# Optimization experiments

Measured on AMD Instinct MI355X. Metric: run time of the kernel, lower is better.

Reference implementation:

```python
import jax, jax.numpy as jnp
import numpy as np

B, N, C = 2, 2048, 1024
H = 16
D = C // H
HID = 4 * C
EPS = 1e-5


def layernorm(x, g, b):
    mu = jnp.mean(x, axis=-1, keepdims=True)
    var = jnp.var(x, axis=-1, keepdims=True)
    return (x - mu) * jax.lax.rsqrt(var + EPS) * g + b


def setup_inputs() -> dict:
    key = jax.random.key(0)
    ks = jax.random.split(key, 8)
    s = lambda fan_in: 1.0 / np.sqrt(fan_in)
    return {
        "x": jax.random.normal(ks[0], (B, N, C), dtype=jnp.float32),
        "ln1_g": jnp.ones((C,), jnp.float32),
        "ln1_b": jnp.zeros((C,), jnp.float32),
        "w_qkv": jax.random.normal(ks[1], (C, 3 * C), jnp.float32) * s(C),
        "w_proj": jax.random.normal(ks[2], (C, C), jnp.float32) * s(C),
        "b_proj": jnp.zeros((C,), jnp.float32),
        "ln2_g": jnp.ones((C,), jnp.float32),
        "ln2_b": jnp.zeros((C,), jnp.float32),
        "w_fc1": jax.random.normal(ks[3], (C, HID), jnp.float32) * s(C),
        "b_fc1": jnp.zeros((HID,), jnp.float32),
        "w_fc2": jax.random.normal(ks[4], (HID, C), jnp.float32) * s(HID),
        "b_fc2": jnp.zeros((C,), jnp.float32),
        "metadata": 0,
        "thw_shape": 2048,
    }


def reference(x, ln1_g, ln1_b, w_qkv, w_proj, b_proj, ln2_g, ln2_b,
              w_fc1, b_fc1, w_fc2, b_fc2, metadata, thw_shape):
    scale = 1.0 / np.sqrt(D)
    # --- attention branch (pre-norm) ---
    xn = layernorm(x, ln1_g, ln1_b)
    qkv = (xn @ w_qkv).reshape(B, N, 3, H, D)
    q = jnp.transpose(qkv[:, :, 0], (0, 2, 1, 3))  # [B,H,N,D]
    k = jnp.transpose(qkv[:, :, 1], (0, 2, 1, 3))
    v = jnp.transpose(qkv[:, :, 2], (0, 2, 1, 3))
    attn = jax.nn.softmax(jnp.einsum('bhnd,bhmd->bhnm', q, k) * scale, axis=-1)
    o = jnp.einsum('bhnm,bhmd->bhnd', attn, v)
    o = jnp.transpose(o, (0, 2, 1, 3)).reshape(B, N, C)
    x = x + (o @ w_proj + b_proj)
    # --- MLP branch (pre-norm) ---
    xn2 = layernorm(x, ln2_g, ln2_b)
    h = jax.nn.gelu(xn2 @ w_fc1 + b_fc1, approximate=False)  # torch GELU = exact erf
    x = x + (h @ w_fc2 + b_fc2)
    return x
```

## Files before the change

### kernel.cpp

```cpp
#include <hip/hip_runtime.h>

#define B_   2
#define N_   2048
#define C_   1024
#define H_   16
#define D_   64
#define HID_ 4096
#define M_   (B_ * N_)

typedef __attribute__((ext_vector_type(8))) short bf16x8;
typedef __attribute__((ext_vector_type(4))) short short4v;
typedef __attribute__((ext_vector_type(4))) float f32x4;

__device__ __forceinline__ unsigned short f2bf(float f) {
  unsigned int u = __builtin_bit_cast(unsigned int, f);
  u += 0x7fffu + ((u >> 16) & 1u);
  return (unsigned short)(u >> 16);
}

__device__ __forceinline__ void gl2lds16(const void* g, void* l) {
  __builtin_amdgcn_global_load_lds(
      (const __attribute__((address_space(1))) unsigned int*)g,
      (__attribute__((address_space(3))) unsigned int*)l, 16, 0, 0);
}

__global__ __launch_bounds__(256) void ln_kernel(const float* __restrict__ x,
                                                 const float* __restrict__ g,
                                                 const float* __restrict__ bta,
                                                 unsigned short* __restrict__ out) {
  int row  = blockIdx.x * 4 + (threadIdx.x >> 6);
  int lane = threadIdx.x & 63;
  const float* xr = x + (size_t)row * C_;
  float4 v[4];
  float s1 = 0.f, s2 = 0.f;
#pragma unroll
  for (int j = 0; j < 4; j++) {
    v[j] = *(const float4*)(xr + j * 256 + lane * 4);
    s1 += v[j].x + v[j].y + v[j].z + v[j].w;
    s2 += v[j].x * v[j].x + v[j].y * v[j].y + v[j].z * v[j].z + v[j].w * v[j].w;
  }
#pragma unroll
  for (int m = 1; m < 64; m <<= 1) { s1 += __shfl_xor(s1, m); s2 += __shfl_xor(s2, m); }
  float mu  = s1 * (1.0f / C_);
  float var = s2 * (1.0f / C_) - mu * mu;
  float rs  = rsqrtf(var + 1e-5f);
#pragma unroll
  for (int j = 0; j < 4; j++) {
    const float4 gv = *(const float4*)(g + j * 256 + lane * 4);
    const float4 bv = *(const float4*)(bta + j * 256 + lane * 4);
    ushort4 o;
    o.x = f2bf((v[j].x - mu) * rs * gv.x + bv.x);
    o.y = f2bf((v[j].y - mu) * rs * gv.y + bv.y);
    o.z = f2bf((v[j].z - mu) * rs * gv.z + bv.z);
    o.w = f2bf((v[j].w - mu) * rs * gv.w + bv.w);
    *(ushort4*)(out + (size_t)row * C_ + j * 256 + lane * 4) = o;
  }
}

__global__ __launch_bounds__(256) void wtrans_kernel(const float* __restrict__ W,
                                                     unsigned short* __restrict__ Wt,
                                                     int K, int N) {
  __shared__ float t[32][33];
  int n0 = blockIdx.x * 32, k0 = blockIdx.y * 32;
  int tx = threadIdx.x, ty = threadIdx.y;
#pragma unroll
  for (int j = 0; j < 4; j++)
    t[ty + j * 8][tx] = W[(size_t)(k0 + ty + j * 8) * N + n0 + tx];
  __syncthreads();
#pragma unroll
  for (int j = 0; j < 4; j++)
    Wt[(size_t)(n0 + ty + j * 8) * K + k0 + tx] = f2bf(t[tx][ty + j * 8]);
}

__global__ __launch_bounds__(256) void vtrans_kernel(const unsigned short* __restrict__ v,
                                                     unsigned short* __restrict__ vt) {
  __shared__ unsigned short t[32][33];
  int bh = blockIdx.z;
  int n0 = blockIdx.x * 32, d0 = blockIdx.y * 32;
  const unsigned short* src = v + (size_t)bh * N_ * D_;
  unsigned short* dst = vt + (size_t)bh * D_ * N_;
  int tx = threadIdx.x, ty = threadIdx.y;
#pragma unroll
  for (int j = 0; j < 4; j++)
    t[ty + j * 8][tx] = src[(size_t)(n0 + ty + j * 8) * D_ + d0 + tx];
  __syncthreads();
#pragma unroll
  for (int j = 0; j < 4; j++)
    dst[(size_t)(d0 + ty + j * 8) * N_ + n0 + tx] = t[tx][ty + j * 8];
}

template <int MODE, int BN>
__global__ __launch_bounds__(256) void gemm_kernel(
    const unsigned short* __restrict__ A,
    const unsigned short* __restrict__ Wt,
    const float* __restrict__ bias,
    const float* __restrict__ resid,
    float* __restrict__ outf,
    unsigned short* __restrict__ outb0,
    unsigned short* __restrict__ outb1,
    unsigned short* __restrict__ outb2,
    int M, int N, int K) {
  constexpr int MT = (BN == 128) ? 4 : 2;
  __shared__ __align__(16) short As[128][64];
  __shared__ __align__(16) short Bs[BN][64];
  int tid = threadIdx.x;
  int w = tid >> 6, lane = tid & 63, r = lane & 15, quad = lane >> 4;
  int rowbase = (BN == 128) ? (w >> 1) * 64 : w * 32;
  int colbase = (BN == 128) ? (w & 1) * 64 : 0;
  int bM = blockIdx.y * 128, bN = blockIdx.x * BN;

  int srow   = (w << 3) + (lane >> 3);
  int schunk = (lane & 7) ^ ((lane >> 3) & 7);
  const unsigned short* aP = A  + (size_t)(bM + srow) * K + schunk * 8;
  const unsigned short* bP = Wt + (size_t)(bN + srow) * K + schunk * 8;

  int pc0 = (quad ^ (r & 7)) * 8;

  f32x4 acc[MT][4];
#pragma unroll
  for (int i = 0; i < MT; i++)
#pragma unroll
    for (int j = 0; j < 4; j++) acc[i][j] = f32x4{0.f, 0.f, 0.f, 0.f};

  for (int k0 = 0; k0 < K; k0 += 64) {
    __syncthreads();
#pragma unroll
    for (int p = 0; p < 4; p++)
      gl2lds16(aP + (size_t)(p * 32) * K + k0, &As[p * 32 + (w << 3)][0]);
#pragma unroll
    for (int p = 0; p < BN / 32; p++)
      gl2lds16(bP + (size_t)(p * 32) * K + k0, &Bs[p * 32 + (w << 3)][0]);
    __syncthreads();
#pragma unroll
    for (int kh = 0; kh < 2; kh++) {
      int pc = pc0 ^ (kh * 32);
      bf16x8 af[MT], bfr[4];
#pragma unroll
      for (int mt = 0; mt < MT; mt++)
        af[mt] = *(const bf16x8*)&As[rowbase + mt * 16 + r][pc];
#pragma unroll
      for (int nt = 0; nt < 4; nt++)
        bfr[nt] = *(const bf16x8*)&Bs[colbase + nt * 16 + r][pc];
#pragma unroll
      for (int mt = 0; mt < MT; mt++)
#pragma unroll
        for (int nt = 0; nt < 4; nt++)
          acc[mt][nt] = __builtin_amdgcn_mfma_f32_16x16x32_bf16(af[mt], bfr[nt], acc[mt][nt], 0, 0, 0);
    }
  }

#pragma unroll
  for (int mt = 0; mt < MT; mt++) {
#pragma unroll
    for (int nt = 0; nt < 4; nt++) {
#pragma unroll
      for (int i = 0; i < 4; i++) {
        int gm = bM + rowbase + mt * 16 + quad * 4 + i;
        int gn = bN + colbase + nt * 16 + r;
        float val = acc[mt][nt][i];
        if (MODE == 0) {
          int s = gn >> 10, c = gn & 1023;
          int hh = c >> 6, d = c & 63;
          int b = gm >> 11, n = gm & 2047;
          size_t di = ((size_t)(b * H_ + hh) * N_ + n) * D_ + d;
          unsigned short bvv = f2bf(s == 0 ? val * 0.125f : val);
          (s == 0 ? outb0 : (s == 1 ? outb1 : outb2))[di] = bvv;
        } else if (MODE == 1) {
          outf[(size_t)gm * N + gn] = val + bias[gn] + resid[(size_t)gm * N + gn];
        } else {
          float t = val + bias[gn];
          float gl = 0.5f * t * (1.0f + erff(t * 0.70710678118f));
          outb0[(size_t)gm * N + gn] = f2bf(gl);
        }
      }
    }
  }
}

__global__ __launch_bounds__(256) void attn_kernel(const unsigned short* __restrict__ qb,
                                                   const unsigned short* __restrict__ kb,
                                                   const unsigned short* __restrict__ vtb,
                                                   unsigned short* __restrict__ ob) {
  __shared__ __align__(16) short Ks[128][64];
  __shared__ __align__(16) short Vts[64][128];
  int tid = threadIdx.x;
  int w = tid >> 6, lane = tid & 63, r = lane & 15, quad = lane >> 4;
  int bh = blockIdx.x >> 4, qt = blockIdx.x & 15;
  const unsigned short* qh  = qb  + (size_t)bh * N_ * D_;
  const unsigned short* kh  = kb  + (size_t)bh * N_ * D_;
  const unsigned short* vth = vtb + (size_t)bh * D_ * N_;

  bf16x8 qf[2][2];
#pragma unroll
  for (int mt = 0; mt < 2; mt++)
#pragma unroll
    for (int ks = 0; ks < 2; ks++)
      qf[mt][ks] = *(const bf16x8*)(qh + (size_t)(qt * 128 + w * 32 + mt * 16 + r) * D_ + ks * 32 + quad * 8);

  float mst[2] = {-1e30f, -1e30f}, lst[2] = {0.f, 0.f};
  f32x4 oacc[2][4];
#pragma unroll
  for (int mt = 0; mt < 2; mt++)
#pragma unroll
    for (int nt = 0; nt < 4; nt++) oacc[mt][nt] = f32x4{0.f, 0.f, 0.f, 0.f};

  int krow   = (w << 3) + (lane >> 3);
  int kchunk = (lane & 7) ^ ((lane >> 3) & 7);
  const unsigned short* kP = kh + (size_t)krow * D_ + kchunk * 8;
  int vrow   = (w << 2) + (lane >> 4);
  int vchunk = (lane & 15) ^ (vrow & 7);
  const unsigned short* vP = vth + (size_t)vrow * N_ + vchunk * 8;

  short* Plw = &Ks[0][0] + w * 2048;
  int swz = (r & 7);

  for (int t = 0; t < 16; t++) {
    __syncthreads();
#pragma unroll
    for (int p = 0; p < 4; p++)
      gl2lds16(kP + (size_t)(t * 128 + p * 32) * D_, &Ks[p * 32 + (w << 3)][0]);
#pragma unroll
    for (int p = 0; p < 4; p++)
      gl2lds16(vP + (size_t)(p * 16) * N_ + t * 128, &Vts[p * 16 + (w << 2)][0]);
    __syncthreads();

    f32x4 sacc[2][8];
#pragma unroll
    for (int mt = 0; mt < 2; mt++)
#pragma unroll
      for (int nt = 0; nt < 8; nt++) sacc[mt][nt] = f32x4{0.f, 0.f, 0.f, 0.f};
#pragma unroll
    for (int ks = 0; ks < 2; ks++) {
#pragma unroll
      for (int nt = 0; nt < 8; nt++) {
        bf16x8 kfr = *(const bf16x8*)&Ks[nt * 16 + r][((ks * 4 + quad) ^ swz) * 8];
#pragma unroll
        for (int mt = 0; mt < 2; mt++)
          sacc[mt][nt] = __builtin_amdgcn_mfma_f32_16x16x32_bf16(kfr, qf[mt][ks], sacc[mt][nt], 0, 0, 0);
      }
    }

    float alpha[2];
#pragma unroll
    for (int mt = 0; mt < 2; mt++) {
      float tm = -1e30f;
#pragma unroll
      for (int nt = 0; nt < 8; nt++)
#pragma unroll
        for (int i = 0; i < 4; i++) tm = fmaxf(tm, sacc[mt][nt][i]);
      tm = fmaxf(tm, __shfl_xor(tm, 16));
      tm = fmaxf(tm, __shfl_xor(tm, 32));
      float mnew = fmaxf(mst[mt], tm);
      alpha[mt] = __expf(mst[mt] - mnew);
      mst[mt] = mnew;
      float rs = 0.f;
#pragma unroll
      for (int nt = 0; nt < 8; nt++)
#pragma unroll
        for (int i = 0; i < 4; i++) {
          float p = __expf(sacc[mt][nt][i] - mnew);
          sacc[mt][nt][i] = p;
          rs += p;
        }
      rs += __shfl_xor(rs, 16);
      rs += __shfl_xor(rs, 32);
      lst[mt] = lst[mt] * alpha[mt] + rs;
#pragma unroll
      for (int i = 0; i < 4; i++) {
        float av = __shfl(alpha[mt], (lane & 48) | (quad * 4 + i));
#pragma unroll
        for (int nt = 0; nt < 4; nt++) oacc[mt][nt][i] *= av;
      }
    }

    __syncthreads();

#pragma unroll
    for (int mt = 0; mt < 2; mt++) {
#pragma unroll
      for (int nt = 0; nt < 8; nt++) {
        short4v pk;
        pk[0] = (short)f2bf(sacc[mt][nt][0]);
        pk[1] = (short)f2bf(sacc[mt][nt][1]);
        pk[2] = (short)f2bf(sacc[mt][nt][2]);
        pk[3] = (short)f2bf(sacc[mt][nt][3]);
        *(short4v*)&Plw[r * 128 + (((nt * 2 + (quad >> 1)) ^ swz) * 8) + (quad & 1) * 4] = pk;
      }
      asm volatile("" ::: "memory");
#pragma unroll
      for (int ks = 0; ks < 4; ks++) {
        bf16x8 pfr = *(const bf16x8*)&Plw[r * 128 + ((ks * 4 + quad) ^ swz) * 8];
#pragma unroll
        for (int nt2 = 0; nt2 < 4; nt2++) {
          bf16x8 vfr = *(const bf16x8*)&Vts[nt2 * 16 + r][((ks * 4 + quad) ^ swz) * 8];
          oacc[mt][nt2] = __builtin_amdgcn_mfma_f32_16x16x32_bf16(pfr, vfr, oacc[mt][nt2], 0, 0, 0);
        }
      }
      asm volatile("" ::: "memory");
    }
  }

  int bb = bh >> 4, hh = bh & 15;
#pragma unroll
  for (int mt = 0; mt < 2; mt++) {
#pragma unroll
    for (int i = 0; i < 4; i++) {
      float li = __shfl(lst[mt], (lane & 48) | (quad * 4 + i));
      float inv = 1.0f / li;
      int row = qt * 128 + w * 32 + mt * 16 + quad * 4 + i;
#pragma unroll
      for (int nt2 = 0; nt2 < 4; nt2++) {
        int d = nt2 * 16 + r;
        ob[((size_t)bb * N_ + row) * C_ + hh * D_ + d] = f2bf(oacc[mt][nt2][i] * inv);
      }
    }
  }
}

extern "C" void kernel_launch(void* const* d_in, const int* in_sizes, int n_in,
                              void* d_out, int out_size, void* d_ws, size_t ws_size,
                              hipStream_t stream) {
  const float* x     = (const float*)d_in[0];
  const float* ln1g  = (const float*)d_in[1];
  const float* ln1b  = (const float*)d_in[2];
  const float* wqkv  = (const float*)d_in[3];
  const float* wproj = (const float*)d_in[4];
  const float* bproj = (const float*)d_in[5];
  const float* ln2g  = (const float*)d_in[6];
  const float* ln2b  = (const float*)d_in[7];
  const float* wfc1  = (const float*)d_in[8];
  const float* bfc1  = (const float*)d_in[9];
  const float* wfc2  = (const float*)d_in[10];
  const float* bfc2  = (const float*)d_in[11];
  float* out = (float*)d_out;

  const size_t MB = 1u << 20;
  if (ws_size < 88 * MB) return;
  char* w = (char*)d_ws;
  unsigned short* xn    = (unsigned short*)(w + 0 * MB);
  unsigned short* qbuf  = (unsigned short*)(w + 8 * MB);
  unsigned short* kbuf  = (unsigned short*)(w + 16 * MB);
  unsigned short* vbuf  = (unsigned short*)(w + 24 * MB);
  unsigned short* hbuf  = (unsigned short*)(w + 0 * MB);
  unsigned short* obuf  = (unsigned short*)(w + 32 * MB);
  float*          x2    = (float*)         (w + 40 * MB);
  unsigned short* xn2   = (unsigned short*)(w + 56 * MB);
  unsigned short* vtb   = (unsigned short*)(w + 56 * MB);
  unsigned short* wqkvt = (unsigned short*)(w + 64 * MB);
  unsigned short* wprjt = (unsigned short*)(w + 70 * MB);
  unsigned short* wfc1t = (unsigned short*)(w + 72 * MB);
  unsigned short* wfc2t = (unsigned short*)(w + 80 * MB);

  dim3 tb(32, 8);
  ln_kernel<<<M_ / 4, 256, 0, stream>>>(x, ln1g, ln1b, xn);
  wtrans_kernel<<<dim3(3 * C_ / 32, C_ / 32), tb, 0, stream>>>(wqkv, wqkvt, C_, 3 * C_);
  wtrans_kernel<<<dim3(C_ / 32, C_ / 32), tb, 0, stream>>>(wproj, wprjt, C_, C_);
  wtrans_kernel<<<dim3(HID_ / 32, C_ / 32), tb, 0, stream>>>(wfc1, wfc1t, C_, HID_);
  wtrans_kernel<<<dim3(C_ / 32, HID_ / 32), tb, 0, stream>>>(wfc2, wfc2t, HID_, C_);

  gemm_kernel<0, 128><<<dim3(3 * C_ / 128, M_ / 128), 256, 0, stream>>>(
      xn, wqkvt, nullptr, nullptr, nullptr, qbuf, kbuf, vbuf, M_, 3 * C_, C_);
  vtrans_kernel<<<dim3(N_ / 32, D_ / 32, B_ * H_), tb, 0, stream>>>(vbuf, vtb);
  attn_kernel<<<B_ * H_ * (N_ / 128), 256, 0, stream>>>(qbuf, kbuf, vtb, obuf);
  gemm_kernel<1, 64><<<dim3(C_ / 64, M_ / 128), 256, 0, stream>>>(
      obuf, wprjt, bproj, x, x2, nullptr, nullptr, nullptr, M_, C_, C_);
  ln_kernel<<<M_ / 4, 256, 0, stream>>>(x2, ln2g, ln2b, xn2);
  gemm_kernel<2, 128><<<dim3(HID_ / 128, M_ / 128), 256, 0, stream>>>(
      xn2, wfc1t, bfc1, nullptr, nullptr, hbuf, nullptr, nullptr, M_, HID_, C_);
  gemm_kernel<1, 64><<<dim3(C_ / 64, M_ / 128), 256, 0, stream>>>(
      hbuf, wfc2t, bfc2, x2, out, nullptr, nullptr, nullptr, M_, C_, HID_);
}
```

Baseline: 385.8 us.

## Add 256x256-tile 8-wave GEMM with interleaved staging for QKV and FC1

Adds a new GEMM kernel that uses 256x256 output tiles with 512 threads, a double-buffered LDS layout with XOR swizzle, and a schedule that splits global-to-LDS loads into quarter-tiles interleaved with MFMA phases under raised wave priority. The QKV and FC1 projections switch to it. The goal is more data reuse per tile and better overlap of memory loads with matrix math. In exchange the grid gets much smaller (192 and 256 blocks), which can leave CUs underused on a 256-CU part, and register pressure is high with 128 accumulator floats per thread.

```diff
diff --git a/kernel.cpp b/kernel.cpp
--- a/kernel.cpp
+++ b/kernel.cpp
@@ -177,6 +177,175 @@
   }
 }
 
+template <int MODE>
+__global__ __launch_bounds__(512, 2) void gemm256_kernel(
+    const unsigned short* __restrict__ A,
+    const unsigned short* __restrict__ Wt,
+    const float* __restrict__ bias,
+    float* __restrict__ outf,
+    const float* __restrict__ resid,
+    unsigned short* __restrict__ outb0,
+    unsigned short* __restrict__ outb1,
+    unsigned short* __restrict__ outb2,
+    int M, int N, int K) {
+  __shared__ __align__(16) short As[2][256][64];
+  __shared__ __align__(16) short Bs[2][256][64];
+  const int tid = threadIdx.x;
+  const int w = tid >> 6, lane = tid & 63, r = lane & 15, quad = lane >> 4;
+  const int wr = w >> 2, wc = w & 3;
+  const int bN = blockIdx.x * 256, bM = blockIdx.y * 256;
+
+  const int srow   = (w << 3) + (lane >> 3);
+  const int schunk = (lane & 7) ^ ((lane >> 3) & 7);
+  const unsigned short* aSrc = A  + (size_t)(bM + srow) * K + schunk * 8;
+  const unsigned short* bSrc = Wt + (size_t)(bN + srow) * K + schunk * 8;
+  const int wrow = w << 3;
+
+  const int ntiles = K >> 6;
+  const int tmask  = ntiles - 1;
+
+#define STAGE_H(t, h)                                                            \
+  do {                                                                           \
+    int b_ = (t) & 1, tt_ = (t) & tmask;                                         \
+    if ((h) < 2) {                                                               \
+      const unsigned short* p_ = aSrc + (size_t)((h) * 128) * K + tt_ * 64;      \
+      gl2lds16(p_, &As[b_][(h) * 128 + wrow][0]);                                \
+      gl2lds16(p_ + (size_t)64 * K, &As[b_][(h) * 128 + 64 + wrow][0]);          \
+    } else {                                                                     \
+      const unsigned short* p_ = bSrc + (size_t)(((h) - 2) * 128) * K + tt_ * 64;\
+      gl2lds16(p_, &Bs[b_][((h) - 2) * 128 + wrow][0]);                          \
+      gl2lds16(p_ + (size_t)64 * K, &Bs[b_][((h) - 2) * 128 + 64 + wrow][0]);    \
+    }                                                                            \
+  } while (0)
+
+  f32x4 acc[8][4];
+#pragma unroll
+  for (int i = 0; i < 8; i++)
+#pragma unroll
+    for (int j = 0; j < 4; j++) acc[i][j] = f32x4{0.f, 0.f, 0.f, 0.f};
+
+  bf16x8 af[4][2];
+  bf16x8 bfr[4][2];
+
+#define RD_A(b, msub)                                                            \
+  {                                                                              \
+    _Pragma("unroll") for (int mt_ = 0; mt_ < 4; mt_++)                          \
+      _Pragma("unroll") for (int ks_ = 0; ks_ < 2; ks_++)                        \
+        af[mt_][ks_] = *(const bf16x8*)&As[b][wr * 128 + (msub) * 64 + mt_ * 16 + r] \
+                                          [((ks_ * 4 + quad) ^ (r & 7)) * 8];    \
+  }
+#define RD_B(b, nh)                                                              \
+  {                                                                              \
+    _Pragma("unroll") for (int nt_ = 0; nt_ < 2; nt_++)                          \
+      _Pragma("unroll") for (int ks_ = 0; ks_ < 2; ks_++)                        \
+        bfr[(nh) * 2 + nt_][ks_] =                                               \
+            *(const bf16x8*)&Bs[b][wc * 64 + (nh) * 32 + nt_ * 16 + r]           \
+                               [((ks_ * 4 + quad) ^ (r & 7)) * 8];               \
+  }
+#define MM_Q(msub, nh)                                                           \
+  {                                                                              \
+    _Pragma("unroll") for (int mt_ = 0; mt_ < 4; mt_++)                          \
+      _Pragma("unroll") for (int nt_ = 0; nt_ < 2; nt_++)                        \
+        _Pragma("unroll") for (int ks_ = 0; ks_ < 2; ks_++)                      \
+          acc[(msub) * 4 + mt_][(nh) * 2 + nt_] =                                \
+              __builtin_amdgcn_mfma_f32_16x16x32_bf16(                           \
+                  af[mt_][ks_], bfr[(nh) * 2 + nt_][ks_],                        \
+                  acc[(msub) * 4 + mt_][(nh) * 2 + nt_], 0, 0, 0);               \
+  }
+
+#define BARRIER() asm volatile("s_barrier" ::: "memory")
+#define WAITL()   asm volatile("s_waitcnt lgkmcnt(0)" ::: "memory")
+#define WAITV2()  asm volatile("s_waitcnt vmcnt(2)" ::: "memory")
+#define PRIO1()   __builtin_amdgcn_s_setprio(1)
+#define PRIO0()   __builtin_amdgcn_s_setprio(0)
+
+  STAGE_H(0, 0); STAGE_H(0, 1); STAGE_H(0, 2); STAGE_H(0, 3);
+  STAGE_H(1, 0);
+  WAITV2();
+  BARRIER();
+
+  const int niter = ntiles >> 1;
+  for (int i = 0; i < niter; i++) {
+    const int tc = 2 * i;
+    RD_A(0, 0); RD_B(0, 0);
+    STAGE_H(tc + 1, 1);
+    BARRIER(); WAITL();
+    PRIO1(); MM_Q(0, 0); PRIO0();
+    BARRIER();
+    RD_B(0, 1);
+    STAGE_H(tc + 1, 2);
+    BARRIER(); WAITL();
+    PRIO1(); MM_Q(0, 1); PRIO0();
+    BARRIER();
+    RD_A(0, 1);
+    STAGE_H(tc + 1, 3);
+    BARRIER(); WAITL();
+    PRIO1(); MM_Q(1, 1); PRIO0();
+    BARRIER();
+    STAGE_H(tc + 2, 0);
+    BARRIER(); WAITL();
+    PRIO1(); MM_Q(1, 0); PRIO0();
+    WAITV2();
+    BARRIER();
+    RD_A(1, 0); RD_B(1, 0);
+    STAGE_H(tc + 2, 1);
+    BARRIER(); WAITL();
+    PRIO1(); MM_Q(0, 0); PRIO0();
+    BARRIER();
+    RD_B(1, 1);
+    STAGE_H(tc + 2, 2);
+    BARRIER(); WAITL();
+    PRIO1(); MM_Q(0, 1); PRIO0();
+    BARRIER();
+    RD_A(1, 1);
+    STAGE_H(tc + 2, 3);
+    BARRIER(); WAITL();
+    PRIO1(); MM_Q(1, 1); PRIO0();
+    BARRIER();
+    STAGE_H(tc + 3, 0);
+    BARRIER(); WAITL();
+    PRIO1(); MM_Q(1, 0); PRIO0();
+    WAITV2();
+    BARRIER();
+  }
+
+#pragma unroll
+  for (int m = 0; m < 8; m++) {
+#pragma unroll
+    for (int n = 0; n < 4; n++) {
+#pragma unroll
+      for (int i2 = 0; i2 < 4; i2++) {
+        int gm = bM + wr * 128 + m * 16 + quad * 4 + i2;
+        int gn = bN + wc * 64 + n * 16 + r;
+        float val = acc[m][n][i2];
+        if (MODE == 0) {
+          int s = gn >> 10, c = gn & 1023;
+          int hh = c >> 6, d = c & 63;
+          int b = gm >> 11, nn = gm & 2047;
+          size_t di = ((size_t)(b * H_ + hh) * N_ + nn) * D_ + d;
+          unsigned short bvv = f2bf(s == 0 ? val * 0.125f : val);
+          (s == 0 ? outb0 : (s == 1 ? outb1 : outb2))[di] = bvv;
+        } else if (MODE == 1) {
+          outf[(size_t)gm * N + gn] = val + bias[gn] + resid[(size_t)gm * N + gn];
+        } else {
+          float t = val + bias[gn];
+          float gl = 0.5f * t * (1.0f + erff(t * 0.70710678118f));
+          outb0[(size_t)gm * N + gn] = f2bf(gl);
+        }
+      }
+    }
+  }
+#undef STAGE_H
+#undef RD_A
+#undef RD_B
+#undef MM_Q
+#undef BARRIER
+#undef WAITL
+#undef WAITV2
+#undef PRIO1
+#undef PRIO0
+}
+
 __global__ __launch_bounds__(256) void attn_kernel(const unsigned short* __restrict__ qb,
                                                    const unsigned short* __restrict__ kb,
                                                    const unsigned short* __restrict__ vtb,
@@ -358,14 +527,14 @@
   wtrans_kernel<<<dim3(HID_ / 32, C_ / 32), tb, 0, stream>>>(wfc1, wfc1t, C_, HID_);
   wtrans_kernel<<<dim3(C_ / 32, HID_ / 32), tb, 0, stream>>>(wfc2, wfc2t, HID_, C_);
 
-  gemm_kernel<0, 128><<<dim3(3 * C_ / 128, M_ / 128), 256, 0, stream>>>(
+  gemm256_kernel<0><<<dim3(3 * C_ / 256, M_ / 256), 512, 0, stream>>>(
       xn, wqkvt, nullptr, nullptr, nullptr, qbuf, kbuf, vbuf, M_, 3 * C_, C_);
   vtrans_kernel<<<dim3(N_ / 32, D_ / 32, B_ * H_), tb, 0, stream>>>(vbuf, vtb);
   attn_kernel<<<B_ * H_ * (N_ / 128), 256, 0, stream>>>(qbuf, kbuf, vtb, obuf);
   gemm_kernel<1, 64><<<dim3(C_ / 64, M_ / 128), 256, 0, stream>>>(
       obuf, wprjt, bproj, x, x2, nullptr, nullptr, nullptr, M_, C_, C_);
   ln_kernel<<<M_ / 4, 256, 0, stream>>>(x2, ln2g, ln2b, xn2);
-  gemm_kernel<2, 128><<<dim3(HID_ / 128, M_ / 128), 256, 0, stream>>>(
+  gemm256_kernel<2><<<dim3(HID_ / 256, M_ / 256), 512, 0, stream>>>(
       xn2, wfc1t, bfc1, nullptr, nullptr, hbuf, nullptr, nullptr, M_, HID_, C_);
   gemm_kernel<1, 64><<<dim3(C_ / 64, M_ / 128), 256, 0, stream>>>(
       hbuf, wfc2t, bfc2, x2, out, nullptr, nullptr, nullptr, M_, C_, HID_);
```

Result: no change. 384.9 us (-0.2%).
